# Performance work log

Measured on AMD Instinct MI355X. Metric: run time of the kernel, lower is better.

The kernel has to match this reference:

```python
import jax, jax.numpy as jnp
import numpy as np
from jax import lax

RATIO = 0.25
RADIUS = 0.2
NSAMPLE = 32


def _fps(xyz, S):
    # xyz: [B, N, 3] -> indices [B, S] via farthest point sampling (start at 0)
    B, N, _ = xyz.shape

    def body(carry, _):
        dist, farthest = carry  # dist [B,N], farthest [B]
        centroid = jnp.take_along_axis(xyz, farthest[:, None, None], axis=1)  # [B,1,3]
        d = jnp.sum((xyz - centroid) ** 2, axis=-1)  # [B,N]
        dist = jnp.minimum(dist, d)
        nxt = jnp.argmax(dist, axis=-1).astype(jnp.int32)
        return (dist, nxt), farthest

    init = (jnp.full((B, N), 1e10, dtype=xyz.dtype), jnp.zeros((B,), jnp.int32))
    _, idx = lax.scan(body, init, None, length=S)  # [S, B]
    return idx.T  # [B, S]


def _ball_query(radius, nsample, xyz, new_xyz):
    # xyz: [B,N,3], new_xyz: [B,S,3] -> neighbor indices [B,S,nsample]
    B, N, _ = xyz.shape
    sqr = jnp.sum((new_xyz[:, :, None, :] - xyz[:, None, :, :]) ** 2, axis=-1)  # [B,S,N]
    arange = jnp.arange(N, dtype=jnp.int32)[None, None, :]
    idx = jnp.where(sqr <= radius * radius, arange, N)  # out-of-ball -> sentinel N
    idx = jnp.sort(idx, axis=-1)[:, :, :nsample]  # first nsample in-ball points
    first = idx[:, :, :1]
    idx = jnp.where(idx == N, first, idx)  # pad with first valid neighbor
    return idx


def reference(xyz, features, w1, b1, w2, b2, w3, b3):
    # xyz: [B,N,3]; features unused in the non-group_all branch (faithful to source).
    B, N, _ = xyz.shape
    S = int(RATIO * N)

    fps_idx = _fps(xyz, S)  # [B,S]
    new_xyz = jnp.take_along_axis(xyz, fps_idx[:, :, None], axis=1)  # [B,S,3]

    nbr_idx = _ball_query(RADIUS, NSAMPLE, xyz, new_xyz)  # [B,S,K]
    b_idx = jnp.arange(B, dtype=jnp.int32)[:, None, None]
    grouped = xyz[b_idx, nbr_idx]  # [B,S,K,3]
    rel = grouped - new_xyz[:, :, None, :]  # center-relative coords

    # new_points.permute(0,3,2,1): [B,S,K,C] -> [B,C,K,S]; shared 1x1 conv MLP + ReLU
    x = rel.transpose(0, 3, 2, 1)  # [B,3,K,S]
    x = jax.nn.relu(jnp.einsum('bcks,oc->boks', x, w1) + b1[None, :, None, None])
    x = jax.nn.relu(jnp.einsum('bcks,oc->boks', x, w2) + b2[None, :, None, None])
    x = jax.nn.relu(jnp.einsum('bcks,oc->boks', x, w3) + b3[None, :, None, None])

    new_points = jnp.max(x, axis=2)  # max over nsample -> [B,128,S]
    return new_xyz.transpose(0, 2, 1), new_points  # [B,3,S], [B,128,S]


def setup_inputs() -> dict:
    key = jax.random.key(0)
    ks = jax.random.split(key, 8)
    B, N = 8, 8192
    xyz = jax.random.uniform(ks[0], (B, N, 3), dtype=jnp.float32)
    features = jax.random.normal(ks[1], (B, 64, N), dtype=jnp.float32)
    w1 = jax.random.normal(ks[2], (64, 3), dtype=jnp.float32) * (1.0 / np.sqrt(3))
    b1 = jnp.zeros((64,), jnp.float32)
    w2 = jax.random.normal(ks[3], (64, 64), dtype=jnp.float32) * (1.0 / np.sqrt(64))
    b2 = jnp.zeros((64,), jnp.float32)
    w3 = jax.random.normal(ks[4], (128, 64), dtype=jnp.float32) * (1.0 / np.sqrt(64))
    b3 = jnp.zeros((128,), jnp.float32)
    return {"xyz": xyz, "features": features, "w1": w1, "b1": b1,
            "w2": w2, "b2": b2, "w3": w3, "b3": b3}
```

## Files before the change

### kernel.cpp

```cpp
#include <hip/hip_runtime.h>
#include <cstdint>
#include <cstddef>

#define BB 8
#define NN 8192
#define SS 2048
#define KNB 32

__device__ __forceinline__ float sqdist_exact(float ax, float ay, float az,
                                              float bx, float by, float bz) {
#pragma clang fp contract(off)
    float dx = ax - bx;
    float dy = ay - by;
    float dz = az - bz;
    return (dx * dx + dy * dy) + dz * dz;
}

template <int CTRL>
__device__ __forceinline__ float dpp_fmax_step(float x) {
    int t = __builtin_amdgcn_update_dpp(__float_as_int(-1.0f), __float_as_int(x),
                                        CTRL, 0xf, 0xf, false);
    return fmaxf(x, __int_as_float(t));
}
template <int CTRL>
__device__ __forceinline__ int dpp_imin_step(int x) {
    int t = __builtin_amdgcn_update_dpp(0x7fffffff, x, CTRL, 0xf, 0xf, false);
    return min(x, t);
}
template <int CTRL>
__device__ __forceinline__ unsigned long long dpp_u64max_step(unsigned long long k) {
    int lo = __builtin_amdgcn_update_dpp(0, (int)(unsigned)(k & 0xffffffffu),
                                         CTRL, 0xf, 0xf, false);
    int hi = __builtin_amdgcn_update_dpp(0, (int)(unsigned)(k >> 32),
                                         CTRL, 0xf, 0xf, false);
    unsigned long long o = ((unsigned long long)(unsigned)hi << 32) | (unsigned)lo;
    return (o > k) ? o : k;
}
#define ROW_SHR1 0x111
#define ROW_SHR2 0x112
#define ROW_SHR4 0x114
#define ROW_SHR8 0x118
#define ROW_BC15 0x142
#define ROW_BC31 0x143

__global__ void prep_kernel(const float* __restrict__ w1, const float* __restrict__ w2,
                            const float* __restrict__ w3, float* __restrict__ w1T,
                            float* __restrict__ w2T, float* __restrict__ w3T) {
    for (int i = threadIdx.x; i < 192; i += 256) {
        int oc = i / 3, c = i % 3;
        w1T[c * 64 + oc] = w1[i];
    }
    for (int i = threadIdx.x; i < 4096; i += 256) {
        int oc = i >> 6, j = i & 63;
        w2T[j * 64 + oc] = w2[i];
    }
    for (int i = threadIdx.x; i < 8192; i += 256) {
        int oc = i >> 6, j = i & 63;
        w3T[j * 128 + oc] = w3[i];
    }
}

__device__ __forceinline__ int part3(int v) {
    return (v & 1) | ((v & 2) << 2) | ((v & 4) << 4);
}

#define PT_LIST(X) X(0) X(1) X(2) X(3) X(4) X(5) X(6) X(7) \
                   X(8) X(9) X(10) X(11) X(12) X(13) X(14) X(15)

__global__ __attribute__((amdgpu_flat_work_group_size(512, 512),
                          amdgpu_waves_per_eu(2, 2)))
void fps_kernel(const float* __restrict__ xyz_all,
                float4* __restrict__ wsSorted,
                float4* __restrict__ wsCtr,
                float* __restrict__ out0) {
    const int b = blockIdx.x;
    const float* xyz = xyz_all + (size_t)b * NN * 3;
    float4* sorted = wsSorted + (size_t)b * NN;
    float4* ctr = wsCtr + (size_t)b * SS;
    float* o0 = out0 + (size_t)b * 3 * SS;

    __shared__ float xLds[NN];
    __shared__ float yLds[NN];
    __shared__ float zLds[NN];
    __shared__ float4 ctrLds[SS];
    __shared__ int cellCnt[512];
    __shared__ int cellBase[512];
    __shared__ unsigned long long red[2][8];

    const int tid = threadIdx.x;
    const int wid = tid >> 6;
    const int lane = tid & 63;

    cellCnt[tid] = 0;
    __syncthreads();
    int cellReg[16];
#pragma unroll
    for (int j = 0; j < 16; ++j) {
        int p = tid + j * 512;
        float x = xyz[p * 3 + 0], y = xyz[p * 3 + 1], z = xyz[p * 3 + 2];
        xLds[p] = x; yLds[p] = y; zLds[p] = z;
        int qx = min(7, (int)(x * 8.0f));
        int qy = min(7, (int)(y * 8.0f));
        int qz = min(7, (int)(z * 8.0f));
        cellReg[j] = part3(qx) | (part3(qy) << 1) | (part3(qz) << 2);
        atomicAdd(&cellCnt[cellReg[j]], 1);
    }
    __syncthreads();
    int myCnt = cellCnt[tid];
    for (int off = 1; off < 512; off <<= 1) {
        int v = (tid >= off) ? cellCnt[tid - off] : 0;
        __syncthreads();
        cellCnt[tid] += v;
        __syncthreads();
    }
    cellBase[tid] = cellCnt[tid] - myCnt;
    __syncthreads();
#pragma unroll
    for (int j = 0; j < 16; ++j) {
        int p = tid + j * 512;
        float x = xLds[p], y = yLds[p], z = zLds[p];
        int pos = atomicAdd(&cellBase[cellReg[j]], 1);
        sorted[(pos & 15) * 512 + (pos >> 4)] = make_float4(x, y, z, __int_as_float(p));
    }
    __threadfence();
    __syncthreads();

    float lox = 1e30f, loy = 1e30f, loz = 1e30f;
    float hix = -1e30f, hiy = -1e30f, hiz = -1e30f;
#define DECL_PT(i)                          \
    float px##i, py##i, pz##i, dist##i;     \
    int od##i;                              \
    {                                       \
        float4 v = sorted[i * 512 + tid];   \
        px##i = v.x; py##i = v.y; pz##i = v.z; \
        od##i = __float_as_int(v.w);        \
        dist##i = 1e10f;                    \
        lox = fminf(lox, v.x); hix = fmaxf(hix, v.x); \
        loy = fminf(loy, v.y); hiy = fmaxf(hiy, v.y); \
        loz = fminf(loz, v.z); hiz = fmaxf(hiz, v.z); \
    }
    PT_LIST(DECL_PT)

    float wlox = lox, wloy = loy, wloz = loz, whix = hix, whiy = hiy, whiz = hiz;
#pragma unroll
    for (int off = 1; off < 64; off <<= 1) {
        wlox = fminf(wlox, __shfl_xor(wlox, off));
        wloy = fminf(wloy, __shfl_xor(wloy, off));
        wloz = fminf(wloz, __shfl_xor(wloz, off));
        whix = fmaxf(whix, __shfl_xor(whix, off));
        whiy = fmaxf(whiy, __shfl_xor(whiy, off));
        whiz = fmaxf(whiz, __shfl_xor(whiz, off));
    }

    float cx = xLds[0], cy = yLds[0], cz = zLds[0];
    if (tid == 0) ctrLds[0] = make_float4(cx, cy, cz, 0.0f);

    unsigned long long waveKey =
        ((unsigned long long)__float_as_uint(1e10f) << 32) | 0xFFFFFFFFull;
    float wave_bv = 1e10f;

    for (int s = 1; s < SS; ++s) {
        const int par = s & 1;
        float ddx = fmaxf(fmaxf(wlox - cx, cx - whix), 0.0f);
        float ddy = fmaxf(fmaxf(wloy - cy, cy - whiy), 0.0f);
        float ddz = fmaxf(fmaxf(wloz - cz, cz - whiz), 0.0f);
        float lb2 = ddx * ddx + ddy * ddy + ddz * ddz;
        if (lb2 * 0.999f < wave_bv) {
            float nbv = -1.0f;
#define UPD_PT(i)                                                        \
    {                                                                    \
        float d = sqdist_exact(px##i, py##i, pz##i, cx, cy, cz);         \
        dist##i = fminf(dist##i, d);                                     \
        nbv = fmaxf(nbv, dist##i);                                       \
    }
            PT_LIST(UPD_PT)
            float m = nbv;
            m = dpp_fmax_step<ROW_SHR1>(m);
            m = dpp_fmax_step<ROW_SHR2>(m);
            m = dpp_fmax_step<ROW_SHR4>(m);
            m = dpp_fmax_step<ROW_SHR8>(m);
            m = dpp_fmax_step<ROW_BC15>(m);
            m = dpp_fmax_step<ROW_BC31>(m);
            float wv = __int_as_float(__builtin_amdgcn_readlane(__float_as_int(m), 63));
            int cand = 0x7fffffff;
#define IDX_PT(i) cand = (dist##i == wv) ? min(cand, od##i) : cand;
            PT_LIST(IDX_PT)
            cand = dpp_imin_step<ROW_SHR1>(cand);
            cand = dpp_imin_step<ROW_SHR2>(cand);
            cand = dpp_imin_step<ROW_SHR4>(cand);
            cand = dpp_imin_step<ROW_SHR8>(cand);
            cand = dpp_imin_step<ROW_BC15>(cand);
            cand = dpp_imin_step<ROW_BC31>(cand);
            int wiw = __builtin_amdgcn_readlane(cand, 63);
            waveKey = ((unsigned long long)__float_as_uint(wv) << 32) |
                      (unsigned)(~(unsigned)wiw);
            wave_bv = wv;
        }
        if (lane == 0) red[par][wid] = waveKey;
        __syncthreads();
        unsigned long long k = red[par][lane & 7];
        k = dpp_u64max_step<ROW_SHR1>(k);
        k = dpp_u64max_step<ROW_SHR2>(k);
        k = dpp_u64max_step<ROW_SHR4>(k);
        unsigned blo = (unsigned)__builtin_amdgcn_readlane(
            (int)(unsigned)(k & 0xffffffffu), 7);
        int wiu = (int)(~blo);
        cx = xLds[wiu];
        cy = yLds[wiu];
        cz = zLds[wiu];
        if (tid == 0) ctrLds[s] = make_float4(cx, cy, cz, 0.0f);
    }

    __syncthreads();
    for (int s = tid; s < SS; s += 512) {
        float4 c = ctrLds[s];
        o0[s] = c.x;
        o0[SS + s] = c.y;
        o0[2 * SS + s] = c.z;
        ctr[s] = c;
    }
}

__global__ __launch_bounds__(128) void bqmlp_kernel(const float* __restrict__ xyz_all,
                                                    const float4* __restrict__ wsCtr,
                                                    const float* __restrict__ w1T,
                                                    const float* __restrict__ b1,
                                                    const float* __restrict__ w2T,
                                                    const float* __restrict__ b2,
                                                    const float* __restrict__ w3T,
                                                    const float* __restrict__ b3,
                                                    float* __restrict__ out1) {
    const int b = blockIdx.x >> 10;
    const int s0 = (blockIdx.x & 1023) * 2;
    const float* xyz = xyz_all + (size_t)b * NN * 3;

    __shared__ float relF[2 * KNB * 3];
    __shared__ float hT[64 * 64];

    const int tid = threadIdx.x;
    const int cb = __builtin_amdgcn_readfirstlane(tid >> 6);
    const int l = tid & 63;

    {
        float4 cc = wsCtr[(size_t)b * SS + s0 + cb];
        float ccx = cc.x, ccy = cc.y, ccz = cc.z;
        const float R2 = (float)(0.2 * 0.2);
        int total = 0;
        float fx = 0.f, fy = 0.f, fz = 0.f;
        bool have = false;
        for (int chunk = 0; chunk < 128 && total < KNB; ++chunk) {
            int p = chunk * 64 + l;
            float x = xyz[p * 3 + 0], y = xyz[p * 3 + 1], z = xyz[p * 3 + 2];
            float d = sqdist_exact(ccx, ccy, ccz, x, y, z);
            bool hit = (d <= R2);
            unsigned long long mask = __ballot(hit);
            int cnt = __popcll(mask);
            if (cnt) {
                int pos = total + __popcll(mask & ((1ull << l) - 1ull));
                float rx = x - ccx, ry = y - ccy, rz = z - ccz;
                if (hit && pos < KNB) {
                    relF[(cb * KNB + pos) * 3 + 0] = rx;
                    relF[(cb * KNB + pos) * 3 + 1] = ry;
                    relF[(cb * KNB + pos) * 3 + 2] = rz;
                }
                if (hit && pos == 0) { fx = rx; fy = ry; fz = rz; have = true; }
                total += cnt;
            }
        }
        unsigned long long hm = __ballot(have);
        if (total < KNB) {
            int src = __ffsll((long long)hm) - 1;
            float gx = __shfl(fx, src), gy = __shfl(fy, src), gz = __shfl(fz, src);
            if (l >= total && l < KNB) {
                relF[(cb * KNB + l) * 3 + 0] = gx;
                relF[(cb * KNB + l) * 3 + 1] = gy;
                relF[(cb * KNB + l) * 3 + 2] = gz;
            }
        }
    }
    __syncthreads();

    const int r = l;

    {
        float rx = relF[r * 3 + 0], ry = relF[r * 3 + 1], rz = relF[r * 3 + 2];
#pragma unroll
        for (int i = 0; i < 32; ++i) {
            int ch = cb * 32 + i;
            float h = b1[ch];
            h = fmaf(rx, w1T[0 * 64 + ch], h);
            h = fmaf(ry, w1T[1 * 64 + ch], h);
            h = fmaf(rz, w1T[2 * 64 + ch], h);
            hT[ch * 64 + r] = fmaxf(h, 0.0f);
        }
    }
    __syncthreads();

    {
        float acc[32];
#pragma unroll
        for (int i = 0; i < 32; ++i) acc[i] = b2[cb * 32 + i];
#pragma unroll 4
        for (int j = 0; j < 64; ++j) {
            float a = hT[j * 64 + r];
            const float* wrow = w2T + j * 64 + cb * 32;
#pragma unroll
            for (int i = 0; i < 32; ++i) acc[i] = fmaf(a, wrow[i], acc[i]);
        }
        __syncthreads();
#pragma unroll
        for (int i = 0; i < 32; ++i) hT[(cb * 32 + i) * 64 + r] = fmaxf(acc[i], 0.0f);
    }
    __syncthreads();

    {
        float acc[64];
#pragma unroll
        for (int i = 0; i < 64; ++i) acc[i] = b3[cb * 64 + i];
#pragma unroll 2
        for (int j = 0; j < 64; ++j) {
            float a = hT[j * 64 + r];
            const float* wrow = w3T + j * 128 + cb * 64;
#pragma unroll
            for (int i = 0; i < 64; ++i) acc[i] = fmaf(a, wrow[i], acc[i]);
        }
#pragma unroll
        for (int i = 0; i < 64; ++i) {
            float v = fmaxf(acc[i], 0.0f);
            v = fmaxf(v, __shfl_xor(v, 1));
            v = fmaxf(v, __shfl_xor(v, 2));
            v = fmaxf(v, __shfl_xor(v, 4));
            v = fmaxf(v, __shfl_xor(v, 8));
            v = fmaxf(v, __shfl_xor(v, 16));
            acc[i] = v;
        }
        if ((l & 31) == 0) {
            int sA = s0 + (l >> 5);
            float* op = out1 + ((size_t)b * 128 + cb * 64) * SS + sA;
#pragma unroll
            for (int i = 0; i < 64; ++i) op[(size_t)i * SS] = acc[i];
        }
    }
}

extern "C" void kernel_launch(void* const* d_in, const int* in_sizes, int n_in,
                              void* d_out, int out_size, void* d_ws, size_t ws_size,
                              hipStream_t stream) {
    (void)in_sizes; (void)n_in; (void)out_size; (void)ws_size;
    const float* xyz = (const float*)d_in[0];
    const float* w1 = (const float*)d_in[2];
    const float* b1 = (const float*)d_in[3];
    const float* w2 = (const float*)d_in[4];
    const float* b2 = (const float*)d_in[5];
    const float* w3 = (const float*)d_in[6];
    const float* b3 = (const float*)d_in[7];
    float* out = (float*)d_out;

    float4* wsCtr = (float4*)d_ws;
    float4* wsSorted = wsCtr + BB * SS;
    float* w1T = (float*)(wsSorted + BB * NN);
    float* w2T = w1T + 192;
    float* w3T = w2T + 4096;

    prep_kernel<<<1, 256, 0, stream>>>(w1, w2, w3, w1T, w2T, w3T);
    fps_kernel<<<BB, 512, 0, stream>>>(xyz, wsSorted, wsCtr, out);
    bqmlp_kernel<<<BB * (SS / 2), 128, 0, stream>>>(xyz, wsCtr, w1T, b1, w2T, b2,
                                                    w3T, b3, out + BB * 3 * SS);
}
```

Baseline: 2.010 ms.

## Use per-register brick bounding boxes to skip FPS distance updates

Points are now stored in Morton-sorted contiguous bricks of 64, one brick per register slot per wave, and each brick gets its own wave-uniform bounding box held in one lane. Each FPS iteration tests all 16 brick boxes against the current centroid, ballots the result, and updates distances only for bricks that could still change the wave maximum. This replaces a single wave-wide bounding box check with finer-grained culling, cutting the per-iteration distance work. In exchange it adds a ballot, readfirstlane and per-brick branches to every iteration, and the per-brick box setup costs many more shuffles.

```diff
diff --git a/kernel.cpp b/kernel.cpp
--- a/kernel.cpp
+++ b/kernel.cpp
@@ -42,6 +42,17 @@
 #define ROW_SHR8 0x118
 #define ROW_BC15 0x142
 #define ROW_BC31 0x143
+
+__device__ __forceinline__ void wave_minmax(float x, float& lo, float& hi) {
+    float a = x, b = x;
+#pragma unroll
+    for (int off = 1; off < 64; off <<= 1) {
+        a = fminf(a, __shfl_xor(a, off));
+        b = fmaxf(b, __shfl_xor(b, off));
+    }
+    lo = a;
+    hi = b;
+}
 
 __global__ void prep_kernel(const float* __restrict__ w1, const float* __restrict__ w2,
                             const float* __restrict__ w3, float* __restrict__ w1T,
@@ -120,37 +131,37 @@
         int p = tid + j * 512;
         float x = xLds[p], y = yLds[p], z = zLds[p];
         int pos = atomicAdd(&cellBase[cellReg[j]], 1);
-        sorted[(pos & 15) * 512 + (pos >> 4)] = make_float4(x, y, z, __int_as_float(p));
+        sorted[pos] = make_float4(x, y, z, __int_as_float(p));
     }
     __threadfence();
     __syncthreads();
 
-    float lox = 1e30f, loy = 1e30f, loz = 1e30f;
-    float hix = -1e30f, hiy = -1e30f, hiz = -1e30f;
-#define DECL_PT(i)                          \
-    float px##i, py##i, pz##i, dist##i;     \
-    int od##i;                              \
-    {                                       \
-        float4 v = sorted[i * 512 + tid];   \
-        px##i = v.x; py##i = v.y; pz##i = v.z; \
-        od##i = __float_as_int(v.w);        \
-        dist##i = 1e10f;                    \
-        lox = fminf(lox, v.x); hix = fmaxf(hix, v.x); \
-        loy = fminf(loy, v.y); hiy = fmaxf(hiy, v.y); \
-        loz = fminf(loz, v.z); hiz = fmaxf(hiz, v.z); \
+#define DECL_PT(i)                                      \
+    float px##i, py##i, pz##i, dist##i;                 \
+    int od##i;                                          \
+    {                                                   \
+        float4 v = sorted[(wid * 16 + i) * 64 + lane];  \
+        px##i = v.x; py##i = v.y; pz##i = v.z;          \
+        od##i = __float_as_int(v.w);                    \
+        dist##i = 1e10f;                                \
     }
     PT_LIST(DECL_PT)
 
-    float wlox = lox, wloy = loy, wloz = loz, whix = hix, whiy = hiy, whiz = hiz;
-#pragma unroll
-    for (int off = 1; off < 64; off <<= 1) {
-        wlox = fminf(wlox, __shfl_xor(wlox, off));
-        wloy = fminf(wloy, __shfl_xor(wloy, off));
-        wloz = fminf(wloz, __shfl_xor(wloz, off));
-        whix = fmaxf(whix, __shfl_xor(whix, off));
-        whiy = fmaxf(whiy, __shfl_xor(whiy, off));
-        whiz = fmaxf(whiz, __shfl_xor(whiz, off));
-    }
+    float bbxlo = 0.f, bbxhi = 0.f, bbylo = 0.f, bbyhi = 0.f,
+          bbzlo = 0.f, bbzhi = 0.f;
+#define BRICK_BB(i)                                               \
+    {                                                             \
+        float xl, xh, yl, yh, zl, zh;                             \
+        wave_minmax(px##i, xl, xh);                               \
+        wave_minmax(py##i, yl, yh);                               \
+        wave_minmax(pz##i, zl, zh);                               \
+        if (lane == i) {                                          \
+            bbxlo = xl; bbxhi = xh;                               \
+            bbylo = yl; bbyhi = yh;                               \
+            bbzlo = zl; bbzhi = zh;                               \
+        }                                                         \
+    }
+    PT_LIST(BRICK_BB)
 
     float cx = xLds[0], cy = yLds[0], cz = zLds[0];
     if (tid == 0) ctrLds[0] = make_float4(cx, cy, cz, 0.0f);
@@ -161,19 +172,23 @@
 
     for (int s = 1; s < SS; ++s) {
         const int par = s & 1;
-        float ddx = fmaxf(fmaxf(wlox - cx, cx - whix), 0.0f);
-        float ddy = fmaxf(fmaxf(wloy - cy, cy - whiy), 0.0f);
-        float ddz = fmaxf(fmaxf(wloz - cz, cz - whiz), 0.0f);
-        float lb2 = ddx * ddx + ddy * ddy + ddz * ddz;
-        if (lb2 * 0.999f < wave_bv) {
+        float ddx = fmaxf(fmaxf(bbxlo - cx, cx - bbxhi), 0.0f);
+        float ddy = fmaxf(fmaxf(bbylo - cy, cy - bbyhi), 0.0f);
+        float ddz = fmaxf(fmaxf(bbzlo - cz, cz - bbzhi), 0.0f);
+        float lb2 = (ddx * ddx + ddy * ddy) + ddz * ddz;
+        bool act = (lane < 16) && (lb2 * 0.999f < wave_bv);
+        unsigned mask = (unsigned)__builtin_amdgcn_readfirstlane(
+            (int)(unsigned)__ballot(act));
+        if (mask) {
+#define UPD_BR(i)                                                     \
+    if (mask & (1u << i)) {                                           \
+        float d = sqdist_exact(px##i, py##i, pz##i, cx, cy, cz);      \
+        dist##i = fminf(dist##i, d);                                  \
+    }
+            PT_LIST(UPD_BR)
             float nbv = -1.0f;
-#define UPD_PT(i)                                                        \
-    {                                                                    \
-        float d = sqdist_exact(px##i, py##i, pz##i, cx, cy, cz);         \
-        dist##i = fminf(dist##i, d);                                     \
-        nbv = fmaxf(nbv, dist##i);                                       \
-    }
-            PT_LIST(UPD_PT)
+#define NBV_PT(i) nbv = fmaxf(nbv, dist##i);
+            PT_LIST(NBV_PT)
             float m = nbv;
             m = dpp_fmax_step<ROW_SHR1>(m);
             m = dpp_fmax_step<ROW_SHR2>(m);
```

Result: no change. 1.998 ms (-0.6%).
